# Kernel optimization log

Measured on AMD Instinct MI355X. Metric: run time of the kernel, lower is better.

## Reference

```python
import jax, jax.numpy as jnp
import numpy as np

BETA = 0.95
THR = 1.0
SLOPE = 25.0


@jax.custom_vjp
def spike(x):
    # Heaviside spike with fast-sigmoid surrogate gradient (snntorch fast_sigmoid, slope=25)
    return (x > 0).astype(x.dtype)

def _spike_fwd(x):
    return spike(x), x

def _spike_bwd(x, g):
    sg = 1.0 / (SLOPE * jnp.abs(x) + 1.0) ** 2
    return (g * sg,)

spike.defvjp(_spike_fwd, _spike_bwd)


def setup_inputs() -> dict:
    key = jax.random.key(0)
    k_x, k_w1, k_b1, k_w2, k_b2 = jax.random.split(key, 5)
    T, B, D_IN, H, OUT = 30, 4096, 784, 128, 10
    x = jax.random.uniform(k_x, (T, B, D_IN), dtype=jnp.float32)
    # PyTorch nn.Linear default init: U(-1/sqrt(fan_in), 1/sqrt(fan_in))
    lim1 = 1.0 / np.sqrt(D_IN)
    lim2 = 1.0 / np.sqrt(H)
    W1 = jax.random.uniform(k_w1, (H, D_IN), jnp.float32, -lim1, lim1)
    b1 = jax.random.uniform(k_b1, (H,), jnp.float32, -lim1, lim1)
    W2 = jax.random.uniform(k_w2, (OUT, H), jnp.float32, -lim2, lim2)
    b2 = jax.random.uniform(k_b2, (OUT,), jnp.float32, -lim2, lim2)
    return {"x": x, "W1": W1, "b1": b1, "W2": W2, "b2": b2}


def reference(x, W1, b1, W2, b2):
    T, B, _ = x.shape
    H, OUT = W1.shape[0], W2.shape[0]

    def step(carry, xt):
        mem1, mem2 = carry
        # layer 1: linear + leaky integrate-and-fire (reset by subtraction)
        cur1 = xt @ W1.T + b1  # [B, H]
        reset1 = jax.lax.stop_gradient((mem1 - THR > 0).astype(xt.dtype))
        mem1 = BETA * mem1 + cur1 - reset1 * THR
        spk1 = spike(mem1 - THR)
        # layer 2
        cur2 = spk1 @ W2.T + b2  # [B, OUT]
        reset2 = jax.lax.stop_gradient((mem2 - THR > 0).astype(xt.dtype))
        mem2 = BETA * mem2 + cur2 - reset2 * THR
        spk2 = spike(mem2 - THR)
        return (mem1, mem2), (spk2, mem2)

    init = (jnp.zeros((B, H), x.dtype), jnp.zeros((B, OUT), x.dtype))
    _, (spk2_rec, mem2_rec) = jax.lax.scan(step, init, x)
    return spk2_rec, mem2_rec  # each [T, B, OUT]
```

## Files before the change

kernel.cpp:

```cpp
#include <hip/hip_runtime.h>
#include <stdint.h>

#define THR  1.0f
#define BETA 0.95f
#define SX   4096.0f
#define SW   512.0f
#define SINV (1.0f / (4096.0f * 512.0f))
#define W1N  (128 * 784)

typedef __attribute__((ext_vector_type(8)))  _Float16 f16x8;
typedef __attribute__((ext_vector_type(16))) float    f32x16;
typedef __attribute__((ext_vector_type(4)))  float    fvec4;

__device__ __forceinline__ void gll16(const float* g, float* l){
  __builtin_amdgcn_global_load_lds((const __attribute__((address_space(1))) void*)g,
                                   (__attribute__((address_space(3))) void*)l, 16, 0, 0);
}

__global__ void split_w1(const float* __restrict__ W1, _Float16* __restrict__ wB){
  int i = blockIdx.x * 256 + threadIdx.x;
  if (i < W1N) {
    int h = i / 784, k = i % 784;
    float v = W1[i] * SW;
    _Float16 hi = (_Float16)v;
    _Float16 lo = (_Float16)(v - (float)hi);
    int ks = k >> 4, kg = (k >> 3) & 1, j = k & 7, nf = h >> 5, r = h & 31;
    int base = ((ks * 4 + nf) * 2) * 512 + (kg * 32 + r) * 8 + j;
    wB[base]       = hi;
    wB[base + 512] = lo;
  }
}

__launch_bounds__(256, 2)
__global__ void gemm1(const float* __restrict__ x,
                      const float* __restrict__ wBf,
                      const float* __restrict__ b1,
                      float* __restrict__ cur1,
                      long row0){
  __shared__ float lds[20480];
  const int lane = threadIdx.x & 63;
  const int w    = threadIdx.x >> 6;
  const long blk_row0 = row0 + (long)blockIdx.x * 128;
  const int r  = lane & 31;
  const int kg = lane >> 5;

  const float* xA = x + (blk_row0 + w * 32 + r) * 784 + kg * 8;

  #define STAGE(p, s) {                                                      \
    _Pragma("unroll") for (int ksl = 0; ksl < 2; ++ksl) {                    \
      gll16(xA + (s) * 32 + ksl * 16,                                        \
            &lds[(p) * 4096 + w * 1024 + ksl * 512]);                        \
      gll16(xA + (s) * 32 + ksl * 16 + 4,                                    \
            &lds[(p) * 4096 + w * 1024 + ksl * 512 + 256]); }                \
    _Pragma("unroll") for (int i = 0; i < 4; ++i) {                          \
      int j = w * 4 + i;                                                     \
      gll16(wBf + (s) * 4096 + j * 256 + lane * 4,                           \
            &lds[8192 + (p) * 4096 + j * 256]); } }

  #define KSTEP(p, ksl) {                                                    \
    f16x8 b[8];                                                              \
    _Pragma("unroll") for (int f = 0; f < 8; ++f)                            \
      b[f] = *(const f16x8*)&lds[8192 + (p) * 4096 + ((ksl) * 8 + f) * 256 + lane * 4]; \
    fvec4 a0 = *(const fvec4*)&lds[(p) * 4096 + w * 1024 + (ksl) * 512 + lane * 4]; \
    fvec4 a1 = *(const fvec4*)&lds[(p) * 4096 + w * 1024 + (ksl) * 512 + 256 + lane * 4]; \
    f16x8 ah, al;                                                            \
    _Pragma("unroll") for (int j = 0; j < 8; ++j) {                          \
      float v = ((j < 4) ? a0[j] : a1[j - 4]) * SX;                          \
      _Float16 hh = (_Float16)v;                                             \
      ah[j] = hh; al[j] = (_Float16)(v - (float)hh);                         \
    }                                                                        \
    _Pragma("unroll") for (int nf = 0; nf < 4; ++nf) {                       \
      acc[nf] = __builtin_amdgcn_mfma_f32_32x32x16_f16(ah, b[nf * 2],     acc[nf], 0, 0, 0); \
      acc[nf] = __builtin_amdgcn_mfma_f32_32x32x16_f16(ah, b[nf * 2 + 1], acc[nf], 0, 0, 0); \
      acc[nf] = __builtin_amdgcn_mfma_f32_32x32x16_f16(al, b[nf * 2],     acc[nf], 0, 0, 0); \
    } }

  #define CPH(p) { KSTEP(p, 0); KSTEP(p, 1); }

  #define VMB(vm) {                                                          \
    asm volatile("s_waitcnt vmcnt(" #vm ")" ::: "memory");                   \
    __builtin_amdgcn_s_barrier();                                            \
    asm volatile("" ::: "memory");                                           \
    __builtin_amdgcn_sched_barrier(0); }

  f32x16 acc[4] = {};

  gll16(xA + 768,     &lds[16384 + w * 512]);
  gll16(xA + 768 + 4, &lds[16384 + w * 512 + 256]);
  #pragma unroll
  for (int i = 0; i < 2; ++i) {
    int j = w * 2 + i;
    gll16(wBf + 98304 + j * 256 + lane * 4, &lds[18432 + j * 256]);
  }
  STAGE(0, 0);

  for (int q = 0; q < 11; ++q) {
    const int s = 2 * q;
    STAGE(1, s + 1); VMB(8); CPH(0);
    STAGE(0, s + 2); VMB(8); CPH(1);
  }
  STAGE(1, 23); VMB(8); CPH(0);
  VMB(0); CPH(1);

  {
    f16x8 b[8];
    #pragma unroll
    for (int f = 0; f < 8; ++f)
      b[f] = *(const f16x8*)&lds[18432 + f * 256 + lane * 4];
    fvec4 a0 = *(const fvec4*)&lds[16384 + w * 512 + lane * 4];
    fvec4 a1 = *(const fvec4*)&lds[16384 + w * 512 + 256 + lane * 4];
    f16x8 ah, al;
    #pragma unroll
    for (int j = 0; j < 8; ++j) {
      float v = ((j < 4) ? a0[j] : a1[j - 4]) * SX;
      _Float16 hh = (_Float16)v;
      ah[j] = hh; al[j] = (_Float16)(v - (float)hh);
    }
    #pragma unroll
    for (int nf = 0; nf < 4; ++nf) {
      acc[nf] = __builtin_amdgcn_mfma_f32_32x32x16_f16(ah, b[nf * 2],     acc[nf], 0, 0, 0);
      acc[nf] = __builtin_amdgcn_mfma_f32_32x32x16_f16(ah, b[nf * 2 + 1], acc[nf], 0, 0, 0);
      acc[nf] = __builtin_amdgcn_mfma_f32_32x32x16_f16(al, b[nf * 2],     acc[nf], 0, 0, 0);
    }
  }

  float b1v[4];
  #pragma unroll
  for (int nf = 0; nf < 4; ++nf) b1v[nf] = b1[nf * 32 + r];
  long m0 = (long)blockIdx.x * 128 + w * 32;
  #pragma unroll
  for (int nf = 0; nf < 4; ++nf)
    #pragma unroll
    for (int reg = 0; reg < 16; ++reg) {
      int rr = (reg & 3) + 8 * (reg >> 2) + 4 * kg;
      cur1[(m0 + rr) * 128 + nf * 32 + r] = acc[nf][reg] * SINV + b1v[nf];
    }
  #undef STAGE
  #undef KSTEP
  #undef CPH
  #undef VMB
}

__launch_bounds__(256)
__global__ void lif(const float* __restrict__ cur1,
                    const float* __restrict__ W2,
                    const float* __restrict__ b2,
                    float* __restrict__ out,
                    float* __restrict__ state1,
                    float* __restrict__ state2,
                    int t0, int tn){
  const int lane = threadIdx.x & 63;
  const int b = blockIdx.x * 4 + (threadIdx.x >> 6);
  const int o = lane & 15;
  const int c = lane >> 4;

  float wv[32];
  #pragma unroll
  for (int j = 0; j < 32; ++j) wv[j] = 0.f;
  if (o < 10) {
    #pragma unroll
    for (int j = 0; j < 32; ++j) wv[j] = W2[o * 128 + c * 32 + j];
  }
  float b2v = (lane < 10) ? b2[lane] : 0.f;

  float mem1a, mem1b, mem2;
  if (t0 == 0) { mem1a = 0.f; mem1b = 0.f; mem2 = 0.f; }
  else {
    mem1a = state1[b * 128 + lane];
    mem1b = state1[b * 128 + 64 + lane];
    mem2  = (lane < 10) ? state2[b * 10 + lane] : 0.f;
  }

  for (int t = t0; t < tn; ++t) {
    long base = ((long)(t - t0) * 4096 + b) * 128;
    float c1a = cur1[base + lane];
    float c1b = cur1[base + 64 + lane];
    float r1a = (mem1a > THR) ? THR : 0.f;
    float r1b = (mem1b > THR) ? THR : 0.f;
    mem1a = BETA * mem1a + c1a - r1a;
    mem1b = BETA * mem1b + c1b - r1b;

    uint64_t mA = __ballot(mem1a > THR);
    uint64_t mB = __ballot(mem1b > THR);
    uint64_t m64 = (c & 2) ? mB : mA;
    uint32_t bits = (uint32_t)(m64 >> ((c & 1) << 5));

    float s = 0.f;
    #pragma unroll
    for (int j = 0; j < 32; ++j)
      s = fmaf((float)((bits >> j) & 1u), wv[j], s);
    s += __shfl_xor(s, 16);
    s += __shfl_xor(s, 32);

    if (lane < 10) {
      float cur2 = s + b2v;
      float r2 = (mem2 > THR) ? THR : 0.f;
      mem2 = BETA * mem2 + cur2 - r2;
      float s2 = (mem2 > THR) ? 1.f : 0.f;
      long ob = (long)t * 40960 + (long)b * 10 + lane;
      out[ob] = s2;
      out[1228800 + ob] = mem2;
    }
  }

  if (tn < 30) {
    state1[b * 128 + lane] = mem1a;
    state1[b * 128 + 64 + lane] = mem1b;
    if (lane < 10) state2[b * 10 + lane] = mem2;
  }
}

extern "C" void kernel_launch(void* const* d_in, const int* in_sizes, int n_in,
                              void* d_out, int out_size, void* d_ws, size_t ws_size,
                              hipStream_t stream) {
  const float* x  = (const float*)d_in[0];
  const float* W1 = (const float*)d_in[1];
  const float* b1 = (const float*)d_in[2];
  const float* W2 = (const float*)d_in[3];
  const float* b2 = (const float*)d_in[4];
  float* out = (float*)d_out;

  const int T = 30, B = 4096;

  char* ws = (char*)d_ws;
  _Float16* wB = (_Float16*)ws;
  size_t off = (size_t)49 * 8 * 512 * sizeof(_Float16);
  off = (off + 255) & ~(size_t)255;
  float* state1 = (float*)(ws + off); off += (size_t)B * 128 * 4;
  float* state2 = (float*)(ws + off); off += (size_t)B * 10 * 4;
  off = (off + 255) & ~(size_t)255;
  float* cur1 = (float*)(ws + off);

  size_t per_t = (size_t)B * 128 * 4;
  size_t avail = (ws_size > off) ? (ws_size - off) : 0;
  int CH = (int)(avail / per_t);
  if (CH > T) CH = T;
  if (CH < 1) CH = 1;

  split_w1<<<(W1N + 255) / 256, 256, 0, stream>>>(W1, wB);

  for (int t0 = 0; t0 < T; t0 += CH) {
    int tn = (t0 + CH < T) ? (t0 + CH) : T;
    int mrows = (tn - t0) * B;
    gemm1<<<mrows / 128, 256, 0, stream>>>(x, (const float*)wB, b1, cur1, (long)t0 * B);
    lif<<<B / 4, 256, 0, stream>>>(cur1, W2, b2, out, state1, state2, t0, tn);
  }
}
```

Measured before the change: 155.8 us.

## Load W1 fragments directly into registers instead of staging through LDS

The split fp16 W1 B-fragments are now read straight from global memory (L2-resident) into double-buffered registers, one fragment per lane, rather than being copied into LDS via global_load_lds and read back. LDS usage halves and the LDS read traffic for B goes away, leaving only the x tiles staged in shared memory. The cost is 32 extra f16x8 registers per thread and redundant global/L2 reads of W1 by every wave, which may pressure occupancy at launch_bounds(256,2) and change the vmcnt wait accounting.

```diff
diff --git a/kernel.cpp b/kernel.cpp
--- a/kernel.cpp
+++ b/kernel.cpp
@@ -33,11 +33,11 @@
 
 __launch_bounds__(256, 2)
 __global__ void gemm1(const float* __restrict__ x,
-                      const float* __restrict__ wBf,
+                      const _Float16* __restrict__ wB,
                       const float* __restrict__ b1,
                       float* __restrict__ cur1,
                       long row0){
-  __shared__ float lds[20480];
+  __shared__ float lds[10240];
   const int lane = threadIdx.x & 63;
   const int w    = threadIdx.x >> 6;
   const long blk_row0 = row0 + (long)blockIdx.x * 128;
@@ -45,70 +45,62 @@
   const int kg = lane >> 5;
 
   const float* xA = x + (blk_row0 + w * 32 + r) * 784 + kg * 8;
-
-  #define STAGE(p, s) {                                                      \
-    _Pragma("unroll") for (int ksl = 0; ksl < 2; ++ksl) {                    \
+  const f16x8* wv = (const f16x8*)wB + lane;
+
+  #define STAGE_A(p, s) { _Pragma("unroll") for (int ksl = 0; ksl < 2; ++ksl) { \
       gll16(xA + (s) * 32 + ksl * 16,                                        \
             &lds[(p) * 4096 + w * 1024 + ksl * 512]);                        \
       gll16(xA + (s) * 32 + ksl * 16 + 4,                                    \
-            &lds[(p) * 4096 + w * 1024 + ksl * 512 + 256]); }                \
-    _Pragma("unroll") for (int i = 0; i < 4; ++i) {                          \
-      int j = w * 4 + i;                                                     \
-      gll16(wBf + (s) * 4096 + j * 256 + lane * 4,                           \
-            &lds[8192 + (p) * 4096 + j * 256]); } }
-
-  #define KSTEP(p, ksl) {                                                    \
-    f16x8 b[8];                                                              \
-    _Pragma("unroll") for (int f = 0; f < 8; ++f)                            \
-      b[f] = *(const f16x8*)&lds[8192 + (p) * 4096 + ((ksl) * 8 + f) * 256 + lane * 4]; \
+            &lds[(p) * 4096 + w * 1024 + ksl * 512 + 256]); } }
+
+  #define LDB(dst, s) { _Pragma("unroll") for (int f = 0; f < 16; ++f)       \
+      dst[f] = wv[((s) * 16 + f) * 64]; }
+
+  #define VMB(vm) {                                                         \
+    asm volatile("s_waitcnt vmcnt(" #vm ")" ::: "memory");                  \
+    __builtin_amdgcn_s_barrier();                                           \
+    asm volatile("" ::: "memory");                                          \
+    __builtin_amdgcn_sched_barrier(0); }
+
+  #define KSTEP(p, breg, ksl) {                                             \
     fvec4 a0 = *(const fvec4*)&lds[(p) * 4096 + w * 1024 + (ksl) * 512 + lane * 4]; \
     fvec4 a1 = *(const fvec4*)&lds[(p) * 4096 + w * 1024 + (ksl) * 512 + 256 + lane * 4]; \
-    f16x8 ah, al;                                                            \
-    _Pragma("unroll") for (int j = 0; j < 8; ++j) {                          \
-      float v = ((j < 4) ? a0[j] : a1[j - 4]) * SX;                          \
-      _Float16 hh = (_Float16)v;                                             \
-      ah[j] = hh; al[j] = (_Float16)(v - (float)hh);                         \
-    }                                                                        \
-    _Pragma("unroll") for (int nf = 0; nf < 4; ++nf) {                       \
-      acc[nf] = __builtin_amdgcn_mfma_f32_32x32x16_f16(ah, b[nf * 2],     acc[nf], 0, 0, 0); \
-      acc[nf] = __builtin_amdgcn_mfma_f32_32x32x16_f16(ah, b[nf * 2 + 1], acc[nf], 0, 0, 0); \
-      acc[nf] = __builtin_amdgcn_mfma_f32_32x32x16_f16(al, b[nf * 2],     acc[nf], 0, 0, 0); \
+    f16x8 ah, al;                                                           \
+    _Pragma("unroll") for (int j = 0; j < 8; ++j) {                         \
+      float v = ((j < 4) ? a0[j] : a1[j - 4]) * SX;                         \
+      _Float16 hh = (_Float16)v;                                            \
+      ah[j] = hh; al[j] = (_Float16)(v - (float)hh);                        \
+    }                                                                       \
+    _Pragma("unroll") for (int nf = 0; nf < 4; ++nf) {                      \
+      acc[nf] = __builtin_amdgcn_mfma_f32_32x32x16_f16(ah, breg[(ksl) * 8 + nf * 2],     acc[nf], 0, 0, 0); \
+      acc[nf] = __builtin_amdgcn_mfma_f32_32x32x16_f16(ah, breg[(ksl) * 8 + nf * 2 + 1], acc[nf], 0, 0, 0); \
+      acc[nf] = __builtin_amdgcn_mfma_f32_32x32x16_f16(al, breg[(ksl) * 8 + nf * 2],     acc[nf], 0, 0, 0); \
     } }
 
-  #define CPH(p) { KSTEP(p, 0); KSTEP(p, 1); }
-
-  #define VMB(vm) {                                                          \
-    asm volatile("s_waitcnt vmcnt(" #vm ")" ::: "memory");                   \
-    __builtin_amdgcn_s_barrier();                                            \
-    asm volatile("" ::: "memory");                                           \
-    __builtin_amdgcn_sched_barrier(0); }
+  #define CPH(p, breg) { KSTEP(p, breg, 0); KSTEP(p, breg, 1); }
 
   f32x16 acc[4] = {};
-
-  gll16(xA + 768,     &lds[16384 + w * 512]);
-  gll16(xA + 768 + 4, &lds[16384 + w * 512 + 256]);
-  #pragma unroll
-  for (int i = 0; i < 2; ++i) {
-    int j = w * 2 + i;
-    gll16(wBf + 98304 + j * 256 + lane * 4, &lds[18432 + j * 256]);
-  }
-  STAGE(0, 0);
+  f16x8 bA[16], bB[16];
+
+  LDB(bA, 0);
+  STAGE_A(0, 0);
+  gll16(xA + 768,     &lds[8192 + w * 512]);
+  gll16(xA + 768 + 4, &lds[8192 + w * 512 + 256]);
 
   for (int q = 0; q < 11; ++q) {
     const int s = 2 * q;
-    STAGE(1, s + 1); VMB(8); CPH(0);
-    STAGE(0, s + 2); VMB(8); CPH(1);
-  }
-  STAGE(1, 23); VMB(8); CPH(0);
-  VMB(0); CPH(1);
-
+    LDB(bB, s + 1); STAGE_A(1, s + 1); VMB(20); CPH(0, bA);
+    LDB(bA, s + 2); STAGE_A(0, s + 2); VMB(20); CPH(1, bB);
+  }
+  LDB(bB, 23); STAGE_A(1, 23); VMB(20); CPH(0, bA);
+  #pragma unroll
+  for (int f = 0; f < 8; ++f) bA[f] = wv[(48 * 8 + f) * 64];
+  VMB(8); CPH(1, bB);
   {
-    f16x8 b[8];
-    #pragma unroll
-    for (int f = 0; f < 8; ++f)
-      b[f] = *(const f16x8*)&lds[18432 + f * 256 + lane * 4];
-    fvec4 a0 = *(const fvec4*)&lds[16384 + w * 512 + lane * 4];
-    fvec4 a1 = *(const fvec4*)&lds[16384 + w * 512 + 256 + lane * 4];
+    asm volatile("s_waitcnt vmcnt(0)" ::: "memory");
+    __builtin_amdgcn_sched_barrier(0);
+    fvec4 a0 = *(const fvec4*)&lds[8192 + w * 512 + lane * 4];
+    fvec4 a1 = *(const fvec4*)&lds[8192 + w * 512 + 256 + lane * 4];
     f16x8 ah, al;
     #pragma unroll
     for (int j = 0; j < 8; ++j) {
@@ -118,9 +110,9 @@
     }
     #pragma unroll
     for (int nf = 0; nf < 4; ++nf) {
-      acc[nf] = __builtin_amdgcn_mfma_f32_32x32x16_f16(ah, b[nf * 2],     acc[nf], 0, 0, 0);
-      acc[nf] = __builtin_amdgcn_mfma_f32_32x32x16_f16(ah, b[nf * 2 + 1], acc[nf], 0, 0, 0);
-      acc[nf] = __builtin_amdgcn_mfma_f32_32x32x16_f16(al, b[nf * 2],     acc[nf], 0, 0, 0);
+      acc[nf] = __builtin_amdgcn_mfma_f32_32x32x16_f16(ah, bA[nf * 2],     acc[nf], 0, 0, 0);
+      acc[nf] = __builtin_amdgcn_mfma_f32_32x32x16_f16(ah, bA[nf * 2 + 1], acc[nf], 0, 0, 0);
+      acc[nf] = __builtin_amdgcn_mfma_f32_32x32x16_f16(al, bA[nf * 2],     acc[nf], 0, 0, 0);
     }
   }
 
@@ -135,10 +127,11 @@
       int rr = (reg & 3) + 8 * (reg >> 2) + 4 * kg;
       cur1[(m0 + rr) * 128 + nf * 32 + r] = acc[nf][reg] * SINV + b1v[nf];
     }
-  #undef STAGE
+  #undef STAGE_A
+  #undef LDB
+  #undef VMB
   #undef KSTEP
   #undef CPH
-  #undef VMB
 }
 
 __launch_bounds__(256)
@@ -242,7 +235,7 @@
   for (int t0 = 0; t0 < T; t0 += CH) {
     int tn = (t0 + CH < T) ? (t0 + CH) : T;
     int mrows = (tn - t0) * B;
-    gemm1<<<mrows / 128, 256, 0, stream>>>(x, (const float*)wB, b1, cur1, (long)t0 * B);
+    gemm1<<<mrows / 128, 256, 0, stream>>>(x, wB, b1, cur1, (long)t0 * B);
     lif<<<B / 4, 256, 0, stream>>>(cur1, W2, b2, out, state1, state2, t0, tn);
   }
 }
```

Measured after the change: 192.2 us. 1.23x slower.
